# Kernel tuning notes

Hardware: AMD Instinct MI355X
Metric: run time of the kernel (lower is better)

Reference implementation:

```python
import jax, jax.numpy as jnp
import numpy as np

NUM_LATENT = 1024
LATENT_DIM = 256
BETA = 0.25
N_TOKENS = 65536


def setup_inputs() -> dict:
    key = jax.random.key(0)
    k1, k2 = jax.random.split(key)
    latent_embedding = jax.random.normal(k1, (N_TOKENS, LATENT_DIM), dtype=jnp.float32)
    # torch.nn.init.uniform_(codebook, -1/num_latent, 1/num_latent)
    codebook = jax.random.uniform(
        k2, (NUM_LATENT, LATENT_DIM), dtype=jnp.float32,
        minval=-1.0 / NUM_LATENT, maxval=1.0 / NUM_LATENT)
    return {"latent_embedding": latent_embedding, "codebook": codebook}


def reference(latent_embedding, codebook):
    le_det = jax.lax.stop_gradient(latent_embedding)  # [N, D]
    # distances[n,k] = ||z_n||^2 + ||c_k||^2 - 2 z_n . c_k   (z detached, codebook NOT)
    distances = (jnp.sum(le_det ** 2, axis=1, keepdims=True)
                 + jnp.sum(codebook ** 2, axis=1)
                 - 2.0 * jnp.matmul(le_det, codebook.T))  # [N, K]
    encoding_inds = jnp.argmin(distances, axis=1)  # [N]
    # one_hot @ codebook == gather rows of codebook
    quantized_latents = codebook[encoding_inds]  # [N, D]
    num_latent = codebook.shape[0]
    commitment_loss = jnp.mean((jax.lax.stop_gradient(quantized_latents)
                                - latent_embedding) ** 2) * num_latent
    embedding_loss = jnp.mean((quantized_latents - le_det) ** 2) * num_latent
    vq_loss = embedding_loss + commitment_loss * BETA
    probs = jax.nn.softmax(-distances, axis=1)  # [N, K]
    probs = jnp.clip(jnp.mean(probs, axis=0, keepdims=True), 0.001, 0.999)  # [1, K]
    return (quantized_latents, codebook, probs, vq_loss)
```

## Files before the change

### kernel.cpp

```cpp
#include <hip/hip_runtime.h>

#define N_TOK 65536
#define DIM   256
#define K_CODES 1024
#define CB_OFF    16777216
#define PROBS_OFF (16777216 + 262144)
#define LOSS_OFF  (16777216 + 262144 + 1024)
#define TM 64
#define NBLK (N_TOK / TM)

typedef float  f32x4  __attribute__((ext_vector_type(4)));
typedef short  s16x8  __attribute__((ext_vector_type(8)));

__device__ __forceinline__ unsigned short f32_to_bf16(float x) {
    unsigned u = __float_as_uint(x);
    unsigned r = (u + 0x7FFFu + ((u >> 16) & 1u)) >> 16;
    return (unsigned short)r;
}
__device__ __forceinline__ unsigned fkey(float a) {
    unsigned u = __float_as_uint(a);
    unsigned m = (unsigned)(((int)u) >> 31);
    return u ^ (m | 0x80000000u);
}
__device__ __forceinline__ float fkey_inv(unsigned k) {
    unsigned u = (k & 0x80000000u) ? (k ^ 0x80000000u) : ~k;
    return __uint_as_float(u);
}

__device__ __forceinline__ unsigned red16_max_u(unsigned v) {
    unsigned t;
    t = (unsigned)__builtin_amdgcn_update_dpp(0, (int)v, 0xB1,  0xF, 0xF, true); v = v > t ? v : t;
    t = (unsigned)__builtin_amdgcn_update_dpp(0, (int)v, 0x4E,  0xF, 0xF, true); v = v > t ? v : t;
    t = (unsigned)__builtin_amdgcn_update_dpp(0, (int)v, 0x141, 0xF, 0xF, true); v = v > t ? v : t;
    t = (unsigned)__builtin_amdgcn_update_dpp(0, (int)v, 0x140, 0xF, 0xF, true); v = v > t ? v : t;
    return v;
}
__device__ __forceinline__ float red16_sum_f(float v) {
    float t;
    t = __uint_as_float((unsigned)__builtin_amdgcn_update_dpp(0, (int)__float_as_uint(v), 0xB1,  0xF, 0xF, true)); v += t;
    t = __uint_as_float((unsigned)__builtin_amdgcn_update_dpp(0, (int)__float_as_uint(v), 0x4E,  0xF, 0xF, true)); v += t;
    t = __uint_as_float((unsigned)__builtin_amdgcn_update_dpp(0, (int)__float_as_uint(v), 0x141, 0xF, 0xF, true)); v += t;
    t = __uint_as_float((unsigned)__builtin_amdgcn_update_dpp(0, (int)__float_as_uint(v), 0x140, 0xF, 0xF, true)); v += t;
    return v;
}

__global__ __launch_bounds__(512) void k_prep(const float* __restrict__ cb,
                                              float* __restrict__ c2,
                                              unsigned short* __restrict__ cbf,
                                              float* __restrict__ probs_part,
                                              float* __restrict__ lossR,
                                              float* __restrict__ outcb,
                                              int zcount, int nloss, int docopy) {
    const int g  = blockIdx.x;
    const int t  = threadIdx.x;
    const int wv = t >> 6;
    const int ln = t & 63;
    const int l15 = ln & 15, q = ln >> 4;

    const float* zp = cb + (size_t)(g * 16 + l15) * DIM + wv * 32 + q * 8;
    f32x4 z0 = *(const f32x4*)(zp);
    f32x4 z1 = *(const f32x4*)(zp + 4);
    s16x8 a;
    a[0] = (short)f32_to_bf16(z0[0]); a[1] = (short)f32_to_bf16(z0[1]);
    a[2] = (short)f32_to_bf16(z0[2]); a[3] = (short)f32_to_bf16(z0[3]);
    a[4] = (short)f32_to_bf16(z1[0]); a[5] = (short)f32_to_bf16(z1[1]);
    a[6] = (short)f32_to_bf16(z1[2]); a[7] = (short)f32_to_bf16(z1[3]);
    *(s16x8*)(cbf + (size_t)(g * 8 + wv) * 1024 + ln * 8) = a;

    float s = z0[0]*z0[0] + z0[1]*z0[1] + z0[2]*z0[2] + z0[3]*z0[3]
            + z1[0]*z1[0] + z1[1]*z1[1] + z1[2]*z1[2] + z1[3]*z1[3];
    s += __shfl_xor(s, 16, 64);
    s += __shfl_xor(s, 32, 64);
    __shared__ float c2p[8][16];
    if (q == 0) c2p[wv][l15] = s;

    const int base = g * 512 + t;
    if (base < nloss) lossR[base] = 0.f;
    if (zcount >= 0) {
        if (base < zcount) probs_part[base] = 0.f;
        if (base + 32768 < zcount) probs_part[base + 32768] = 0.f;
    } else {
        if (base < -zcount) probs_part[(size_t)base * 1024] = 0.f;
    }
    if (docopy) {
        #pragma unroll
        for (int i = 0; i < 8; i++) outcb[base + i * 32768] = cb[base + i * 32768];
    }

    __syncthreads();
    if (t < 16) {
        float acc = 0.f;
        #pragma unroll
        for (int ww = 0; ww < 8; ww++) acc += c2p[ww][t];
        c2[g * 16 + t] = acc;
    }
}

__global__ __launch_bounds__(1024, 4) void k_main(const float* __restrict__ z,
                                                  const float* __restrict__ cb,
                                                  const unsigned short* __restrict__ cbf,
                                                  const float* __restrict__ c2,
                                                  float* __restrict__ out_q,
                                                  float* __restrict__ probs_part,
                                                  float* __restrict__ lossR,
                                                  int repmask) {
    const int t   = threadIdx.x;
    const int w   = t >> 6;
    const int ln  = t & 63;
    const int q   = ln >> 4;
    const int l15 = ln & 15;
    const int k0  = w * 64;
    const int n0  = blockIdx.x * TM;
    float* pp = probs_part +
        (size_t)((repmask < 0) ? (int)blockIdx.x : (int)(blockIdx.x & repmask)) * K_CODES;

    __shared__ unsigned short a_lds[32 * 64 * 8];
    __shared__ float    z2p[32][16];
    __shared__ unsigned kred[16][64];
    __shared__ float    ered[16][64];
    __shared__ int   fidx[64];
    __shared__ float fU[64];

    #pragma unroll
    for (int rep = 0; rep < 2; rep++) {
        const int f   = t + rep * 1024;
        const int md  = w + rep * 16;
        const int m   = md >> 3;
        const int dsv = md & 7;
        const int row = m * 16 + l15;
        const int dim = dsv * 32 + q * 8;
        const float* zp = z + (size_t)(n0 + row) * DIM + dim;
        f32x4 z0 = *(const f32x4*)(zp);
        f32x4 z1 = *(const f32x4*)(zp + 4);
        s16x8 a;
        a[0] = (short)f32_to_bf16(z0[0]); a[1] = (short)f32_to_bf16(z0[1]);
        a[2] = (short)f32_to_bf16(z0[2]); a[3] = (short)f32_to_bf16(z0[3]);
        a[4] = (short)f32_to_bf16(z1[0]); a[5] = (short)f32_to_bf16(z1[1]);
        a[6] = (short)f32_to_bf16(z1[2]); a[7] = (short)f32_to_bf16(z1[3]);
        *(s16x8*)(a_lds + (size_t)f * 8) = a;
        float s = z0[0]*z0[0] + z0[1]*z0[1] + z0[2]*z0[2] + z0[3]*z0[3]
                + z1[0]*z1[0] + z1[1]*z1[1] + z1[2]*z1[2] + z1[3]*z1[3];
        s += __shfl_xor(s, 16, 64);
        s += __shfl_xor(s, 32, 64);
        if (q == 0) z2p[md][l15] = s;
    }

    float c2v[4];
    #pragma unroll
    for (int nt = 0; nt < 4; nt++) c2v[nt] = c2[k0 + nt * 16 + l15];
    f32x4 acc[4][4];
    #pragma unroll
    for (int m = 0; m < 4; m++)
        #pragma unroll
        for (int nt = 0; nt < 4; nt++) {
            const float iv = -0.5f * c2v[nt];
            f32x4 v4 = {iv, iv, iv, iv};
            acc[m][nt] = v4;
        }

    __syncthreads();

    const unsigned short* bb = cbf + (size_t)(w * 4) * 8 * 1024 + ln * 8;
    #pragma unroll
    for (int ds = 0; ds < 8; ds++) {
        s16x8 af[4];
        #pragma unroll
        for (int m = 0; m < 4; m++)
            af[m] = *(const s16x8*)(a_lds + (size_t)((m * 8 + ds) * 64 + ln) * 8);
        #pragma unroll
        for (int nt = 0; nt < 4; nt++) {
            s16x8 b = *(const s16x8*)(bb + (size_t)(nt * 8 + ds) * 1024);
            #pragma unroll
            for (int m = 0; m < 4; m++)
                acc[m][nt] = __builtin_amdgcn_mfma_f32_16x16x32_bf16(af[m], b, acc[m][nt], 0, 0, 0);
        }
    }

    unsigned lkey[4][4];
    float    lesum[4][4];
    #pragma unroll
    for (int m = 0; m < 4; m++)
        #pragma unroll
        for (int v = 0; v < 4; v++) { lkey[m][v] = 0u; lesum[m][v] = 0.f; }

    #pragma unroll
    for (int m = 0; m < 4; m++)
        #pragma unroll
        for (int nt = 0; nt < 4; nt++) {
            const unsigned colc = 1023u - (unsigned)(k0 + nt * 16 + l15);
            #pragma unroll
            for (int v = 0; v < 4; v++) {
                float a = acc[m][nt][v];
                unsigned key = (fkey(a) & 0xFFFFFC00u) | colc;
                lkey[m][v] = max(lkey[m][v], key);
                float e = __expf(a + a);
                acc[m][nt][v] = e;
                lesum[m][v] += e;
            }
        }

    #pragma unroll
    for (int m = 0; m < 4; m++)
        #pragma unroll
        for (int v = 0; v < 4; v++) {
            lkey[m][v]  = red16_max_u(lkey[m][v]);
            lesum[m][v] = red16_sum_f(lesum[m][v]);
        }

    if (l15 == 0) {
        #pragma unroll
        for (int m = 0; m < 4; m++)
            #pragma unroll
            for (int v = 0; v < 4; v++) {
                const int r = m * 16 + q * 4 + v;
                kred[w][r] = lkey[m][v]; ered[w][r] = lesum[m][v];
            }
    }
    __syncthreads();
    float lossreg = 0.f;
    if (t < 64) {
        unsigned bk = kred[0][t];
        float U = ered[0][t];
        #pragma unroll
        for (int ww = 1; ww < 16; ww++) {
            bk = max(bk, kred[ww][t]);
            U += ered[ww][t];
        }
        fidx[t] = 1023 - (int)(bk & 1023u);
        fU[t] = U;
        float a_rec = fkey_inv(bk);
        float z2 = 0.f;
        #pragma unroll
        for (int ds = 0; ds < 8; ds++) z2 += z2p[(t >> 4) * 8 + ds][t & 15];
        lossreg = z2 - 2.0f * a_rec;
    }
    __syncthreads();

    float ps[4];
    #pragma unroll
    for (int nt = 0; nt < 4; nt++) ps[nt] = 0.f;
    #pragma unroll
    for (int m = 0; m < 4; m++)
        #pragma unroll
        for (int v = 0; v < 4; v++) {
            const float invU = 1.0f / fU[m * 16 + q * 4 + v];
            #pragma unroll
            for (int nt = 0; nt < 4; nt++) ps[nt] += acc[m][nt][v] * invU;
        }
    #pragma unroll
    for (int nt = 0; nt < 4; nt++) {
        ps[nt] += __shfl_xor(ps[nt], 16, 64);
        ps[nt] += __shfl_xor(ps[nt], 32, 64);
    }
    if (repmask < 0) pp[k0 + q * 16 + l15] = ps[q];
    else             atomicAdd(&pp[k0 + q * 16 + l15], ps[q]);

    #pragma unroll
    for (int i = 0; i < 4; i++) {
        const int r  = w * 4 + i;
        const int am = fidx[r];
        f32x4 qv = *(const f32x4*)(cb + (size_t)am * DIM + ln * 4);
        *(f32x4*)(out_q + (size_t)(n0 + r) * DIM + ln * 4) = qv;
    }

    if (w == 0) {
        #pragma unroll
        for (int off = 32; off; off >>= 1) lossreg += __shfl_down(lossreg, off, 64);
        if (ln == 0) atomicAdd(&lossR[blockIdx.x & 63], lossreg);
    }
}

__global__ __launch_bounds__(1024) void k_fin(const float* __restrict__ cb,
                                              const float* __restrict__ probs_part,
                                              const float* __restrict__ lossR,
                                              float* __restrict__ out,
                                              int R, int nLoss, int docopy) {
    const int t = threadIdx.x;
    const int g = blockIdx.x * 1024 + t;
    __shared__ float part[16][64];
    if (docopy && g < 262144) out[CB_OFF + g] = cb[g];
    if (R >= NBLK) {
        if (blockIdx.x < 16) {
            const int w  = t >> 6;
            const int ln = t & 63;
            const int col = blockIdx.x * 64 + ln;
            const float* p0 = probs_part + (size_t)(w * 64) * K_CODES + col;
            float a0 = 0.f, a1 = 0.f, a2 = 0.f, a3 = 0.f;
            #pragma unroll 4
            for (int r = 0; r < 64; r += 4) {
                a0 += p0[(size_t)(r + 0) * K_CODES];
                a1 += p0[(size_t)(r + 1) * K_CODES];
                a2 += p0[(size_t)(r + 2) * K_CODES];
                a3 += p0[(size_t)(r + 3) * K_CODES];
            }
            part[w][ln] = a0 + a1 + a2 + a3;
            __syncthreads();
            if (t < 64) {
                float p = 0.f;
                #pragma unroll
                for (int ww = 0; ww < 16; ww++) p += part[ww][t];
                p *= (1.0f / 65536.0f);
                p = fminf(fmaxf(p, 0.001f), 0.999f);
                out[PROBS_OFF + blockIdx.x * 64 + t] = p;
            }
        }
    } else if (g < K_CODES) {
        float a0 = 0.f, a1 = 0.f, a2 = 0.f, a3 = 0.f;
        if (R >= 4) {
            for (int r = 0; r < R; r += 4) {
                a0 += probs_part[(r + 0) * K_CODES + g];
                a1 += probs_part[(r + 1) * K_CODES + g];
                a2 += probs_part[(r + 2) * K_CODES + g];
                a3 += probs_part[(r + 3) * K_CODES + g];
            }
        } else {
            for (int r = 0; r < R; r++) a0 += probs_part[r * K_CODES + g];
        }
        float p = (a0 + a1 + a2 + a3) * (1.0f / 65536.0f);
        p = fminf(fmaxf(p, 0.001f), 0.999f);
        out[PROBS_OFF + g] = p;
    }
    if (g == 0) {
        float ls = 0.f;
        for (int r = 0; r < nLoss; r++) ls += lossR[r];
        out[LOSS_OFF] = ls * (1280.0f / 16777216.0f);
    }
}

extern "C" void kernel_launch(void* const* d_in, const int* in_sizes, int n_in,
                              void* d_out, int out_size, void* d_ws, size_t ws_size,
                              hipStream_t stream) {
    (void)in_sizes; (void)n_in; (void)out_size;
    const float* z  = (const float*)d_in[0];
    const float* cb = (const float*)d_in[1];
    float* out = (float*)d_out;

    float* c2 = (float*)d_ws;

    float *probs_part, *lossR;
    int R, nLoss, repmask;
    size_t used = 1024 * 4;
    auto fits = [&](int r) { return ws_size >= used + (size_t)(64 + r * 1024) * 4; };
    if      (fits(NBLK)) R = NBLK;
    else if (fits(64))   R = 64;
    else if (fits(16))   R = 16;
    else if (fits(4))    R = 4;
    else                 R = 0;
    const int storeMode = (R == NBLK);
    if (R) {
        lossR      = c2 + 1024;
        probs_part = lossR + 64;
        nLoss = 64;
        used += (size_t)(64 + (size_t)R * 1024) * 4;
        repmask = storeMode ? -1 : (R - 1);
    } else {
        probs_part = out + PROBS_OFF;
        lossR      = out + LOSS_OFF;
        R = 1; nLoss = 1; repmask = 0;
    }

    unsigned short* cbf;
    const size_t cbf_bytes = (size_t)512 * 1024 * 2;
    int cbf_in_ws = (ws_size >= used + cbf_bytes);
    if (cbf_in_ws) cbf = (unsigned short*)((char*)d_ws + used);
    else           cbf = (unsigned short*)(out + CB_OFF);

    k_prep<<<dim3(64), dim3(512), 0, stream>>>(cb, c2, cbf, probs_part, lossR,
                                               out + CB_OFF, storeMode ? -NBLK : R * 1024,
                                               nLoss, cbf_in_ws);
    k_main<<<dim3(NBLK), dim3(1024), 0, stream>>>(z, cb, cbf, c2, out, probs_part,
                                                  lossR, repmask);
    const int fin_blocks = (!cbf_in_ws) ? 256 : (storeMode ? 16 : 1);
    k_fin<<<dim3(fin_blocks), dim3(1024), 0, stream>>>(cb, probs_part, lossR, out,
                                                       R, nLoss, !cbf_in_ws);
}
```

Measured before the change: 189.7 us.

## Split z staging: async-load second half to LDS while MFMAs run first half

Only the first half of the latent tile's dimensions is now loaded and converted to bf16 up front. The second half is fetched with global_load_lds into a swizzled fp32 staging buffer and converted after the first four MFMA K-steps, so the global load latency overlaps with matrix work. The change also replaces __expf with a raw exp2 using a folded constant and replaces the division with a hardware reciprocal. In exchange it adds about 32KB of LDS and an extra barrier, which may reduce occupancy.

Measured after the change: 205.3 us. 1.08x slower.

```diff
diff --git a/kernel.cpp b/kernel.cpp
--- a/kernel.cpp
+++ b/kernel.cpp
@@ -42,6 +42,12 @@
     t = __uint_as_float((unsigned)__builtin_amdgcn_update_dpp(0, (int)__float_as_uint(v), 0x141, 0xF, 0xF, true)); v += t;
     t = __uint_as_float((unsigned)__builtin_amdgcn_update_dpp(0, (int)__float_as_uint(v), 0x140, 0xF, 0xF, true)); v += t;
     return v;
+}
+
+__device__ __forceinline__ void gl_lds16(const float* gp, float* lp) {
+    __builtin_amdgcn_global_load_lds(
+        (const __attribute__((address_space(1))) unsigned int*)gp,
+        (__attribute__((address_space(3))) unsigned int*)lp, 16, 0, 0);
 }
 
 __global__ __launch_bounds__(512) void k_prep(const float* __restrict__ cb,
@@ -115,18 +121,28 @@
         (size_t)((repmask < 0) ? (int)blockIdx.x : (int)(blockIdx.x & repmask)) * K_CODES;
 
     __shared__ unsigned short a_lds[32 * 64 * 8];
+    __shared__ float zstage[TM * 128];
     __shared__ float    z2p[32][16];
     __shared__ unsigned kred[16][64];
     __shared__ float    ered[16][64];
     __shared__ int   fidx[64];
     __shared__ float fU[64];
 
-    #pragma unroll
-    for (int rep = 0; rep < 2; rep++) {
-        const int f   = t + rep * 1024;
-        const int md  = w + rep * 16;
-        const int m   = md >> 3;
-        const int dsv = md & 7;
+    {
+        const float* zg = z + (size_t)n0 * DIM + 128;
+        #pragma unroll
+        for (int i = 0; i < 2; i++) {
+            const int r = w * 4 + i * 2 + (ln >> 5);
+            const int f = (ln & 31) * 4;
+            gl_lds16(zg + (size_t)r * DIM + (f ^ ((r & 7) << 2)),
+                     &zstage[(w * 4 + i * 2) * 128]);
+        }
+    }
+
+    {
+        const int m   = w >> 2;
+        const int dsv = w & 3;
+        const int md  = m * 8 + dsv;
         const int row = m * 16 + l15;
         const int dim = dsv * 32 + q * 8;
         const float* zp = z + (size_t)(n0 + row) * DIM + dim;
@@ -137,7 +153,7 @@
         a[2] = (short)f32_to_bf16(z0[2]); a[3] = (short)f32_to_bf16(z0[3]);
         a[4] = (short)f32_to_bf16(z1[0]); a[5] = (short)f32_to_bf16(z1[1]);
         a[6] = (short)f32_to_bf16(z1[2]); a[7] = (short)f32_to_bf16(z1[3]);
-        *(s16x8*)(a_lds + (size_t)f * 8) = a;
+        *(s16x8*)(a_lds + (size_t)(md * 64 + ln) * 8) = a;
         float s = z0[0]*z0[0] + z0[1]*z0[1] + z0[2]*z0[2] + z0[3]*z0[3]
                 + z1[0]*z1[0] + z1[1]*z1[1] + z1[2]*z1[2] + z1[3]*z1[3];
         s += __shfl_xor(s, 16, 64);
@@ -162,7 +178,49 @@
 
     const unsigned short* bb = cbf + (size_t)(w * 4) * 8 * 1024 + ln * 8;
     #pragma unroll
-    for (int ds = 0; ds < 8; ds++) {
+    for (int ds = 0; ds < 4; ds++) {
+        s16x8 af[4];
+        #pragma unroll
+        for (int m = 0; m < 4; m++)
+            af[m] = *(const s16x8*)(a_lds + (size_t)((m * 8 + ds) * 64 + ln) * 8);
+        #pragma unroll
+        for (int nt = 0; nt < 4; nt++) {
+            s16x8 b = *(const s16x8*)(bb + (size_t)(nt * 8 + ds) * 1024);
+            #pragma unroll
+            for (int m = 0; m < 4; m++)
+                acc[m][nt] = __builtin_amdgcn_mfma_f32_16x16x32_bf16(af[m], b, acc[m][nt], 0, 0, 0);
+        }
+    }
+
+    __syncthreads();
+
+    {
+        const int m   = w >> 2;
+        const int dsv = (w & 3) + 4;
+        const int md  = m * 8 + dsv;
+        const int row = m * 16 + l15;
+        const int dl  = (w & 3) * 32 + q * 8;
+        const int sw  = (row & 7) << 2;
+        const float* zp = zstage + row * 128;
+        f32x4 z0 = *(const f32x4*)(zp + (dl ^ sw));
+        f32x4 z1 = *(const f32x4*)(zp + ((dl + 4) ^ sw));
+        s16x8 a;
+        a[0] = (short)f32_to_bf16(z0[0]); a[1] = (short)f32_to_bf16(z0[1]);
+        a[2] = (short)f32_to_bf16(z0[2]); a[3] = (short)f32_to_bf16(z0[3]);
+        a[4] = (short)f32_to_bf16(z1[0]); a[5] = (short)f32_to_bf16(z1[1]);
+        a[6] = (short)f32_to_bf16(z1[2]); a[7] = (short)f32_to_bf16(z1[3]);
+        *(s16x8*)(a_lds + (size_t)(md * 64 + ln) * 8) = a;
+        float s = z0[0]*z0[0] + z0[1]*z0[1] + z0[2]*z0[2] + z0[3]*z0[3]
+                + z1[0]*z1[0] + z1[1]*z1[1] + z1[2]*z1[2] + z1[3]*z1[3];
+        s += __shfl_xor(s, 16, 64);
+        s += __shfl_xor(s, 32, 64);
+        if (q == 0) z2p[md][l15] = s;
+    }
+
+    __syncthreads();
+
+    #pragma unroll
+    for (int ds = 4; ds < 8; ds++) {
         s16x8 af[4];
         #pragma unroll
         for (int m = 0; m < 4; m++)
@@ -193,7 +251,7 @@
                 float a = acc[m][nt][v];
                 unsigned key = (fkey(a) & 0xFFFFFC00u) | colc;
                 lkey[m][v] = max(lkey[m][v], key);
-                float e = __expf(a + a);
+                float e = __builtin_amdgcn_exp2f(a * 2.8853900817779268f);
                 acc[m][nt][v] = e;
                 lesum[m][v] += e;
             }
@@ -243,7 +301,7 @@
     for (int m = 0; m < 4; m++)
         #pragma unroll
         for (int v = 0; v < 4; v++) {
-            const float invU = 1.0f / fU[m * 16 + q * 4 + v];
+            const float invU = __builtin_amdgcn_rcpf(fU[m * 16 + q * 4 + v]);
             #pragma unroll
             for (int nt = 0; nt < 4; nt++) ps[nt] += acc[m][nt][v] * invU;
         }
```
